# Optimization experiments

Hardware: AMD Instinct MI355X
Metric: run time of the kernel (lower is better)

Reference implementation:

```python
import jax, jax.numpy as jnp
import numpy as np

MAX_DELAY = 64   # kernel taps (module default 100; 64 = 4*block_size)
DT = 1.0
K_MIN = 0.1      # floor on storage constant for numerical safety


def _causal_depthwise_conv(x, k):
    """x: [B, C, T], k: [C, Tk].  y[b,c,t] = sum_tau k[c,tau] * x[b,c,t-tau]."""
    Tk = k.shape[1]
    return jax.lax.conv_general_dilated(
        x, k[:, None, ::-1], window_strides=(1,),
        padding=[(Tk - 1, 0)],
        feature_group_count=k.shape[0],
        dimension_numbers=('NCH', 'OIH', 'NCH'))


def _linear_storage_irf(params):
    """Per-node linear-reservoir impulse response, discretized to MAX_DELAY taps.
    params: [N, 2]; uses col 0 as (unconstrained) storage constant. -> [N, Tk]."""
    kst = jax.nn.softplus(params[:, 0]) + K_MIN              # [N]
    t = jnp.arange(MAX_DELAY, dtype=params.dtype) * DT       # [Tk]
    h = jnp.exp(-t[None, :] / kst[:, None]) * (DT / kst[:, None])
    return h / jnp.sum(h, axis=1, keepdims=True)             # unit mass


def setup_inputs() -> dict:
    key = jax.random.key(0)
    k1, k2, k3, k4 = jax.random.split(key, 4)
    B, N, T, E = 2, 4096, 2048, 8192
    x = jax.random.normal(k1, (B, N, T), dtype=jnp.float32)
    params = jax.random.normal(k2, (N, 2), dtype=jnp.float32)
    edge_src = jax.random.randint(k3, (E,), 0, N)
    edge_tgt = jax.random.randint(k4, (E,), 0, N)
    return {"x": x, "params": params, "edge_src": edge_src, "edge_tgt": edge_tgt}


def reference(x, params, edge_src, edge_tgt):
    B, N, T = x.shape
    # --- RoutingIRFAggregator: per-pair routing kernels ---
    h = _linear_storage_irf(params)                 # [N, Tk]
    h_src = h[edge_src]                             # [E, Tk] irregular gather
    h_tgt = h[edge_tgt]                             # [E, Tk]
    # edge kernel = causal composition (convolution) of src and tgt IRFs, truncated to Tk
    K_edge = _causal_depthwise_conv(h_src[None], h_tgt)[0]   # [E, Tk]
    # include diagonal (self) pairs since runoff_to_output=False
    K = jnp.concatenate([K_edge, h], axis=0)                 # [P, Tk], P = E + N
    src_all = jnp.concatenate([edge_src, jnp.arange(N)])
    tgt_all = jnp.concatenate([edge_tgt, jnp.arange(N)])
    # --- BlockSparseCausalConv: per-pair causal conv then scatter-add to targets ---
    xg = x[:, src_all, :]                           # [B, P, T] irregular gather
    yp = _causal_depthwise_conv(xg, K)              # [B, P, T]
    y = jax.ops.segment_sum(yp.transpose(1, 0, 2), tgt_all, num_segments=N)  # [N, B, T]
    return y.transpose(1, 0, 2)                     # [B, N, T]
```

## Files before the change

### kernel.cpp

```cpp
#include <hip/hip_runtime.h>
#include <math.h>

static constexpr int NN = 4096;
static constexpr int TT = 2048;
static constexpr int EE = 8192;
static constexpr int TK = 64;
static constexpr int CAP = 32;

typedef __attribute__((ext_vector_type(8))) short   short8v;
typedef __attribute__((ext_vector_type(4))) float   float4v;

__device__ __forceinline__ unsigned cvtpk_bf16(float lo, float hi) {
    unsigned r;
    asm("v_cvt_pk_bf16_f32 %0, %1, %2" : "=v"(r) : "v"(lo), "v"(hi));
    return r;
}

__global__ void irf_zero_kernel(const float* __restrict__ params,
                                float* __restrict__ hirf, int* __restrict__ cnt) {
    int blk = blockIdx.x;
    if (blk < 1024) {
        int t = blk * 256 + threadIdx.x;
        int node = t >> 6, lane = t & 63;
        float p = params[node * 2];
        float sp = fmaxf(p, 0.f) + log1pf(expf(-fabsf(p)));
        float kst = sp + 0.1f;
        float inv = 1.0f / kst;
        float hv = expf(-(float)lane * inv) * inv;
        float s = hv;
        #pragma unroll
        for (int d = 1; d < 64; d <<= 1) s += __shfl_xor(s, d, 64);
        hirf[node * TK + lane] = hv / s;
    } else {
        int i = (blk - 1024) * 256 + threadIdx.x;
        if (i < NN) cnt[i] = 0;
    }
}

__global__ void kedge_scatter_kernel(const float* __restrict__ hirf,
                                     const int* __restrict__ esrc, const int* __restrict__ etgt,
                                     float* __restrict__ Ke, int* __restrict__ cnt,
                                     int2* __restrict__ elist2) {
    __shared__ float s_src[4][TK];
    __shared__ float s_tgt[4][TK];
    int lane = threadIdx.x & 63;
    int grp  = threadIdx.x >> 6;
    int e = blockIdx.x * 4 + grp;
    int s = esrc[e], t = etgt[e];
    s_src[grp][lane] = hirf[s * TK + lane];
    s_tgt[grp][lane] = hirf[t * TK + lane];
    __syncthreads();
    float acc = 0.f;
    for (int tau = 0; tau <= lane; ++tau)
        acc += s_tgt[grp][tau] * s_src[grp][lane - tau];
    Ke[e * TK + lane] = acc;
    if (lane == 0) {
        int pos = atomicAdd(&cnt[t], 1);
        if (pos < CAP) elist2[t * CAP + pos] = make_int2(e, s);
    }
}

static constexpr int HALO = 80;
static constexpr int XLEN = HALO + TT;
static constexpr int TABS = 96;
static constexpr int TABE = TABS * 16;

struct __align__(16) ConvBuf {
    unsigned short x[XLEN];
    unsigned short tab[TABE];
};

__global__ __launch_bounds__(128)
void conv_mfma_kernel(const float* __restrict__ x,
                      const float* __restrict__ hirf, const float* __restrict__ Ke,
                      const int2* __restrict__ elist2,
                      const int* __restrict__ cnt,
                      float* __restrict__ y) {
    __shared__ ConvBuf sbuf[2];

    const int tid    = threadIdx.x;
    const int bid    = blockIdx.x;
    const int b      = bid & 1;
    const int tgt    = bid >> 1;
    const int l      = tid & 63;
    const int lane16 = l & 15;
    const int h      = l >> 4;
    const int hlo    = h & 1, hhi = h >> 1;
    const int half   = tid >> 6;

    for (int idx = tid; idx < 2 * HALO; idx += 128) {
        int nb = idx / HALO;
        sbuf[nb].x[idx % HALO] = 0;
    }
    {
        int z = tid & 15;
        #pragma unroll
        for (int rr = 0; rr < 2; ++rr) {
            int r2 = (tid >> 4) + 8 * rr;
            int c1 = z, c2 = (z <= r2) ? z + 16 : 80 + z;
            sbuf[0].tab[TABS * r2 + c1] = 0; sbuf[0].tab[TABS * r2 + c2] = 0;
            sbuf[1].tab[TABS * r2 + c1] = 0; sbuf[1].tab[TABS * r2 + c2] = 0;
        }
    }

    float4v acc[4];
    #pragma unroll
    for (int T = 0; T < 4; ++T) acc[T] = (float4v){0.f, 0.f, 0.f, 0.f};

    const float4* xbase = reinterpret_cast<const float4*>(x + (size_t)b * NN * TT);

    float4 pxA[4], pxB[4]; float pkA, pkB;

    auto LOAD_A = [&](int src, const float* Kp) {
        const float4* r0 = xbase + (size_t)src * (TT / 4);
        #pragma unroll
        for (int c = 0; c < 4; ++c) pxA[c] = r0[tid + 128 * c];
        pkA = Kp[l];
    };
    auto LOAD_B = [&](int src, const float* Kp) {
        const float4* r0 = xbase + (size_t)src * (TT / 4);
        #pragma unroll
        for (int c = 0; c < 4; ++c) pxB[c] = r0[tid + 128 * c];
        pkB = Kp[l];
    };
    auto WRITE_A = [&](int nb) {
        #pragma unroll
        for (int c = 0; c < 4; ++c) {
            int u = tid + 128 * c;
            unsigned lo = cvtpk_bf16(pxA[c].x, pxA[c].y);
            unsigned hi = cvtpk_bf16(pxA[c].z, pxA[c].w);
            *reinterpret_cast<uint2*>(&sbuf[nb].x[HALO + 4 * u]) = make_uint2(lo, hi);
        }
        unsigned short kb = (unsigned short)(cvtpk_bf16(pkA, pkA) & 0xffffu);
        int rg = tid >> 6;
        #pragma unroll
        for (int rr = 0; rr < 8; ++rr) {
            int r = rg * 8 + rr;
            sbuf[nb].tab[TABS * r + 80 + r - l] = kb;
        }
    };
    auto WRITE_B = [&](int nb) {
        #pragma unroll
        for (int c = 0; c < 4; ++c) {
            int u = tid + 128 * c;
            unsigned lo = cvtpk_bf16(pxB[c].x, pxB[c].y);
            unsigned hi = cvtpk_bf16(pxB[c].z, pxB[c].w);
            *reinterpret_cast<uint2*>(&sbuf[nb].x[HALO + 4 * u]) = make_uint2(lo, hi);
        }
        unsigned short kb = (unsigned short)(cvtpk_bf16(pkB, pkB) & 0xffffu);
        int rg = tid >> 6;
        #pragma unroll
        for (int rr = 0; rr < 8; ++rr) {
            int r = rg * 8 + rr;
            sbuf[nb].tab[TABS * r + 80 + r - l] = kb;
        }
    };
    auto COMPUTE = [&](int cb) {
        const unsigned short* tab = sbuf[cb].tab;
        const unsigned short* xb  = sbuf[cb].x;
        const int abase = TABS * lane16 + 80 + 8 * hlo;
        short8v A0 = *reinterpret_cast<const short8v*>(&tab[abase - 16 * (0 + hhi)]);
        short8v A1 = *reinterpret_cast<const short8v*>(&tab[abase - 16 * (2 + hhi)]);
        short8v A2 = *reinterpret_cast<const short8v*>(&tab[abase - 16 * (4 + hhi)]);
        #pragma unroll
        for (int T = 0; T < 4; ++T) {
            int bb = HALO + 16 * (64 * half + 16 * T + lane16) + 8 * hlo;
            short8v B0 = *reinterpret_cast<const short8v*>(&xb[bb - 16 * (0 + hhi)]);
            acc[T] = __builtin_amdgcn_mfma_f32_16x16x32_bf16(A0, B0, acc[T], 0, 0, 0);
            short8v B1 = *reinterpret_cast<const short8v*>(&xb[bb - 16 * (2 + hhi)]);
            acc[T] = __builtin_amdgcn_mfma_f32_16x16x32_bf16(A1, B1, acc[T], 0, 0, 0);
            short8v B2 = *reinterpret_cast<const short8v*>(&xb[bb - 16 * (4 + hhi)]);
            acc[T] = __builtin_amdgcn_mfma_f32_16x16x32_bf16(A2, B2, acc[T], 0, 0, 0);
        }
    };

    int deg = __builtin_amdgcn_readfirstlane(cnt[tgt]);
    if (deg > CAP) deg = CAP;
    const int nr = deg + 1;
    int mdE = 0, mdS = 0;

    LOAD_A(tgt, hirf + (size_t)tgt * TK);
    if (nr > 1) {
        int2 m = elist2[tgt * CAP];
        mdE = __builtin_amdgcn_readfirstlane(m.x);
        mdS = __builtin_amdgcn_readfirstlane(m.y);
        LOAD_B(mdS, Ke + (size_t)mdE * TK);
        if (nr > 2) {
            int2 m2 = elist2[tgt * CAP + 1];
            mdE = __builtin_amdgcn_readfirstlane(m2.x);
            mdS = __builtin_amdgcn_readfirstlane(m2.y);
        }
    }
    WRITE_A(0);
    __syncthreads();

    int i = 0;
    while (true) {
        if (i + 2 < nr) {
            LOAD_A(mdS, Ke + (size_t)mdE * TK);
            if (i + 3 < nr) {
                int2 m = elist2[tgt * CAP + i + 2];
                mdE = __builtin_amdgcn_readfirstlane(m.x);
                mdS = __builtin_amdgcn_readfirstlane(m.y);
            }
        }
        COMPUTE(0);
        if (i + 1 >= nr) break;
        WRITE_B(1);
        __syncthreads();
        ++i;
        if (i + 2 < nr) {
            LOAD_B(mdS, Ke + (size_t)mdE * TK);
            if (i + 3 < nr) {
                int2 m = elist2[tgt * CAP + i + 2];
                mdE = __builtin_amdgcn_readfirstlane(m.x);
                mdS = __builtin_amdgcn_readfirstlane(m.y);
            }
        }
        COMPUTE(1);
        if (i + 1 >= nr) break;
        WRITE_A(0);
        __syncthreads();
        ++i;
    }

    float* yrow = y + ((size_t)b * NN + tgt) * TT;
    #pragma unroll
    for (int T = 0; T < 4; ++T) {
        int tb = 16 * (64 * half + 16 * T + lane16) + 4 * h;
        float4v v = acc[T];
        __builtin_nontemporal_store(v, reinterpret_cast<float4v*>(yrow + tb));
    }
}

extern "C" void kernel_launch(void* const* d_in, const int* in_sizes, int n_in,
                              void* d_out, int out_size, void* d_ws, size_t ws_size,
                              hipStream_t stream) {
    const float* x      = (const float*)d_in[0];
    const float* params = (const float*)d_in[1];
    const int*   esrc   = (const int*)d_in[2];
    const int*   etgt   = (const int*)d_in[3];
    float* y = (float*)d_out;

    float* hirf = (float*)d_ws;
    float* Ke   = hirf + (size_t)NN * TK;
    int* cnt      = (int*)(Ke + (size_t)EE * TK);
    int2* elist2  = (int2*)(cnt + NN);

    hipLaunchKernelGGL(irf_zero_kernel, dim3(1040), dim3(256), 0, stream, params, hirf, cnt);
    hipLaunchKernelGGL(kedge_scatter_kernel, dim3(EE / 4), dim3(256), 0, stream,
                       hirf, esrc, etgt, Ke, cnt, elist2);
    hipLaunchKernelGGL(conv_mfma_kernel, dim3(NN * 2), dim3(128), 0, stream,
                       x, hirf, Ke, elist2, cnt, y);
}
```

Measured before the change: 53.85 us.

## Pre-convert x and kernels to bf16 in workspace before the gather conv

Adds a prep pass that converts all of x to bf16 in a workspace buffer, and stores the IRF and edge kernels as bf16. The conv kernel then gathers half-width rows and writes them straight to LDS without converting. Each source row is gathered about three times on average, so halving the gathered bytes is meant to cut memory traffic. The cost is an extra full read of x plus a write of the bf16 copy, and a fallback to fp32 loads if the workspace is too small.

```diff
diff --git a/kernel.cpp b/kernel.cpp
--- a/kernel.cpp
+++ b/kernel.cpp
@@ -7,8 +7,9 @@
 static constexpr int TK = 64;
 static constexpr int CAP = 32;
 
-typedef __attribute__((ext_vector_type(8))) short   short8v;
-typedef __attribute__((ext_vector_type(4))) float   float4v;
+typedef __attribute__((ext_vector_type(8))) short        short8v;
+typedef __attribute__((ext_vector_type(4))) float        float4v;
+typedef __attribute__((ext_vector_type(2))) unsigned int uint2v;
 
 __device__ __forceinline__ unsigned cvtpk_bf16(float lo, float hi) {
     unsigned r;
@@ -16,11 +17,24 @@
     return r;
 }
 
-__global__ void irf_zero_kernel(const float* __restrict__ params,
-                                float* __restrict__ hirf, int* __restrict__ cnt) {
+__global__ void prep_kernel(const float* __restrict__ params,
+                            const float* __restrict__ x,
+                            float* __restrict__ hirf, unsigned short* __restrict__ hb,
+                            unsigned short* __restrict__ xb, int* __restrict__ cnt,
+                            int doX) {
     int blk = blockIdx.x;
     if (blk < 1024) {
-        int t = blk * 256 + threadIdx.x;
+        if (!doX) return;
+        const float4* src = reinterpret_cast<const float4*>(x) + (size_t)blk * 4096 + threadIdx.x;
+        uint2v*       dst = reinterpret_cast<uint2v*>(xb) + (size_t)blk * 4096 + threadIdx.x;
+        #pragma unroll
+        for (int c = 0; c < 16; ++c) {
+            float4 v = src[c * 256];
+            uint2v o; o.x = cvtpk_bf16(v.x, v.y); o.y = cvtpk_bf16(v.z, v.w);
+            dst[c * 256] = o;
+        }
+    } else if (blk < 2048) {
+        int t = (blk - 1024) * 256 + threadIdx.x;
         int node = t >> 6, lane = t & 63;
         float p = params[node * 2];
         float sp = fmaxf(p, 0.f) + log1pf(expf(-fabsf(p)));
@@ -30,17 +44,19 @@
         float s = hv;
         #pragma unroll
         for (int d = 1; d < 64; d <<= 1) s += __shfl_xor(s, d, 64);
-        hirf[node * TK + lane] = hv / s;
+        float val = hv / s;
+        hirf[node * TK + lane] = val;
+        hb[node * TK + lane] = (unsigned short)(cvtpk_bf16(val, val) & 0xffffu);
     } else {
-        int i = (blk - 1024) * 256 + threadIdx.x;
+        int i = (blk - 2048) * 256 + threadIdx.x;
         if (i < NN) cnt[i] = 0;
     }
 }
 
-__global__ void kedge_scatter_kernel(const float* __restrict__ hirf,
-                                     const int* __restrict__ esrc, const int* __restrict__ etgt,
-                                     float* __restrict__ Ke, int* __restrict__ cnt,
-                                     int2* __restrict__ elist2) {
+__global__ void kedge_kernel(const float* __restrict__ hirf,
+                             const int* __restrict__ esrc, const int* __restrict__ etgt,
+                             unsigned short* __restrict__ Kb, int* __restrict__ cnt,
+                             int2* __restrict__ elist2) {
     __shared__ float s_src[4][TK];
     __shared__ float s_tgt[4][TK];
     int lane = threadIdx.x & 63;
@@ -53,7 +69,7 @@
     float acc = 0.f;
     for (int tau = 0; tau <= lane; ++tau)
         acc += s_tgt[grp][tau] * s_src[grp][lane - tau];
-    Ke[e * TK + lane] = acc;
+    Kb[e * TK + lane] = (unsigned short)(cvtpk_bf16(acc, acc) & 0xffffu);
     if (lane == 0) {
         int pos = atomicAdd(&cnt[t], 1);
         if (pos < CAP) elist2[t * CAP + pos] = make_int2(e, s);
@@ -70,9 +86,12 @@
     unsigned short tab[TABE];
 };
 
+template <int BF16X>
 __global__ __launch_bounds__(128)
-void conv_mfma_kernel(const float* __restrict__ x,
-                      const float* __restrict__ hirf, const float* __restrict__ Ke,
+void conv_mfma_kernel(const float* __restrict__ x32,
+                      const unsigned short* __restrict__ xb,
+                      const unsigned short* __restrict__ hb,
+                      const unsigned short* __restrict__ Kb,
                       const int2* __restrict__ elist2,
                       const int* __restrict__ cnt,
                       float* __restrict__ y) {
@@ -107,57 +126,75 @@
     #pragma unroll
     for (int T = 0; T < 4; ++T) acc[T] = (float4v){0.f, 0.f, 0.f, 0.f};
 
-    const float4* xbase = reinterpret_cast<const float4*>(x + (size_t)b * NN * TT);
-
-    float4 pxA[4], pxB[4]; float pkA, pkB;
-
-    auto LOAD_A = [&](int src, const float* Kp) {
-        const float4* r0 = xbase + (size_t)src * (TT / 4);
-        #pragma unroll
-        for (int c = 0; c < 4; ++c) pxA[c] = r0[tid + 128 * c];
+    float4  pxA32[4], pxB32[4];
+    short8v pxA16[2], pxB16[2];
+    unsigned short pkA, pkB;
+
+    auto LOAD_A = [&](int src, const unsigned short* Kp) {
+        if constexpr (BF16X) {
+            const short8v* r = reinterpret_cast<const short8v*>(xb + ((size_t)b * NN + src) * TT);
+            pxA16[0] = r[tid]; pxA16[1] = r[tid + 128];
+        } else {
+            const float4* r = reinterpret_cast<const float4*>(x32 + ((size_t)b * NN + src) * TT);
+            #pragma unroll
+            for (int c = 0; c < 4; ++c) pxA32[c] = r[tid + 128 * c];
+        }
         pkA = Kp[l];
     };
-    auto LOAD_B = [&](int src, const float* Kp) {
-        const float4* r0 = xbase + (size_t)src * (TT / 4);
-        #pragma unroll
-        for (int c = 0; c < 4; ++c) pxB[c] = r0[tid + 128 * c];
+    auto LOAD_B = [&](int src, const unsigned short* Kp) {
+        if constexpr (BF16X) {
+            const short8v* r = reinterpret_cast<const short8v*>(xb + ((size_t)b * NN + src) * TT);
+            pxB16[0] = r[tid]; pxB16[1] = r[tid + 128];
+        } else {
+            const float4* r = reinterpret_cast<const float4*>(x32 + ((size_t)b * NN + src) * TT);
+            #pragma unroll
+            for (int c = 0; c < 4; ++c) pxB32[c] = r[tid + 128 * c];
+        }
         pkB = Kp[l];
     };
     auto WRITE_A = [&](int nb) {
-        #pragma unroll
-        for (int c = 0; c < 4; ++c) {
-            int u = tid + 128 * c;
-            unsigned lo = cvtpk_bf16(pxA[c].x, pxA[c].y);
-            unsigned hi = cvtpk_bf16(pxA[c].z, pxA[c].w);
-            *reinterpret_cast<uint2*>(&sbuf[nb].x[HALO + 4 * u]) = make_uint2(lo, hi);
-        }
-        unsigned short kb = (unsigned short)(cvtpk_bf16(pkA, pkA) & 0xffffu);
+        if constexpr (BF16X) {
+            *reinterpret_cast<short8v*>(&sbuf[nb].x[HALO + 8 * tid])         = pxA16[0];
+            *reinterpret_cast<short8v*>(&sbuf[nb].x[HALO + 8 * (tid + 128)]) = pxA16[1];
+        } else {
+            #pragma unroll
+            for (int c = 0; c < 4; ++c) {
+                int u = tid + 128 * c;
+                unsigned lo = cvtpk_bf16(pxA32[c].x, pxA32[c].y);
+                unsigned hi = cvtpk_bf16(pxA32[c].z, pxA32[c].w);
+                *reinterpret_cast<uint2*>(&sbuf[nb].x[HALO + 4 * u]) = make_uint2(lo, hi);
+            }
+        }
         int rg = tid >> 6;
         #pragma unroll
         for (int rr = 0; rr < 8; ++rr) {
             int r = rg * 8 + rr;
-            sbuf[nb].tab[TABS * r + 80 + r - l] = kb;
+            sbuf[nb].tab[TABS * r + 80 + r - l] = pkA;
         }
     };
     auto WRITE_B = [&](int nb) {
-        #pragma unroll
-        for (int c = 0; c < 4; ++c) {
-            int u = tid + 128 * c;
-            unsigned lo = cvtpk_bf16(pxB[c].x, pxB[c].y);
-            unsigned hi = cvtpk_bf16(pxB[c].z, pxB[c].w);
-            *reinterpret_cast<uint2*>(&sbuf[nb].x[HALO + 4 * u]) = make_uint2(lo, hi);
-        }
-        unsigned short kb = (unsigned short)(cvtpk_bf16(pkB, pkB) & 0xffffu);
+        if constexpr (BF16X) {
+            *reinterpret_cast<short8v*>(&sbuf[nb].x[HALO + 8 * tid])         = pxB16[0];
+            *reinterpret_cast<short8v*>(&sbuf[nb].x[HALO + 8 * (tid + 128)]) = pxB16[1];
+        } else {
+            #pragma unroll
+            for (int c = 0; c < 4; ++c) {
+                int u = tid + 128 * c;
+                unsigned lo = cvtpk_bf16(pxB32[c].x, pxB32[c].y);
+                unsigned hi = cvtpk_bf16(pxB32[c].z, pxB32[c].w);
+                *reinterpret_cast<uint2*>(&sbuf[nb].x[HALO + 4 * u]) = make_uint2(lo, hi);
+            }
+        }
         int rg = tid >> 6;
         #pragma unroll
         for (int rr = 0; rr < 8; ++rr) {
             int r = rg * 8 + rr;
-            sbuf[nb].tab[TABS * r + 80 + r - l] = kb;
+            sbuf[nb].tab[TABS * r + 80 + r - l] = pkB;
         }
     };
     auto COMPUTE = [&](int cb) {
         const unsigned short* tab = sbuf[cb].tab;
-        const unsigned short* xb  = sbuf[cb].x;
+        const unsigned short* xv  = sbuf[cb].x;
         const int abase = TABS * lane16 + 80 + 8 * hlo;
         short8v A0 = *reinterpret_cast<const short8v*>(&tab[abase - 16 * (0 + hhi)]);
         short8v A1 = *reinterpret_cast<const short8v*>(&tab[abase - 16 * (2 + hhi)]);
@@ -165,11 +202,11 @@
         #pragma unroll
         for (int T = 0; T < 4; ++T) {
             int bb = HALO + 16 * (64 * half + 16 * T + lane16) + 8 * hlo;
-            short8v B0 = *reinterpret_cast<const short8v*>(&xb[bb - 16 * (0 + hhi)]);
+            short8v B0 = *reinterpret_cast<const short8v*>(&xv[bb - 16 * (0 + hhi)]);
             acc[T] = __builtin_amdgcn_mfma_f32_16x16x32_bf16(A0, B0, acc[T], 0, 0, 0);
-            short8v B1 = *reinterpret_cast<const short8v*>(&xb[bb - 16 * (2 + hhi)]);
+            short8v B1 = *reinterpret_cast<const short8v*>(&xv[bb - 16 * (2 + hhi)]);
             acc[T] = __builtin_amdgcn_mfma_f32_16x16x32_bf16(A1, B1, acc[T], 0, 0, 0);
-            short8v B2 = *reinterpret_cast<const short8v*>(&xb[bb - 16 * (4 + hhi)]);
+            short8v B2 = *reinterpret_cast<const short8v*>(&xv[bb - 16 * (4 + hhi)]);
             acc[T] = __builtin_amdgcn_mfma_f32_16x16x32_bf16(A2, B2, acc[T], 0, 0, 0);
         }
     };
@@ -179,12 +216,12 @@
     const int nr = deg + 1;
     int mdE = 0, mdS = 0;
 
-    LOAD_A(tgt, hirf + (size_t)tgt * TK);
+    LOAD_A(tgt, hb + (size_t)tgt * TK);
     if (nr > 1) {
         int2 m = elist2[tgt * CAP];
         mdE = __builtin_amdgcn_readfirstlane(m.x);
         mdS = __builtin_amdgcn_readfirstlane(m.y);
-        LOAD_B(mdS, Ke + (size_t)mdE * TK);
+        LOAD_B(mdS, Kb + (size_t)mdE * TK);
         if (nr > 2) {
             int2 m2 = elist2[tgt * CAP + 1];
             mdE = __builtin_amdgcn_readfirstlane(m2.x);
@@ -197,7 +234,7 @@
     int i = 0;
     while (true) {
         if (i + 2 < nr) {
-            LOAD_A(mdS, Ke + (size_t)mdE * TK);
+            LOAD_A(mdS, Kb + (size_t)mdE * TK);
             if (i + 3 < nr) {
                 int2 m = elist2[tgt * CAP + i + 2];
                 mdE = __builtin_amdgcn_readfirstlane(m.x);
@@ -210,7 +247,7 @@
         __syncthreads();
         ++i;
         if (i + 2 < nr) {
-            LOAD_B(mdS, Ke + (size_t)mdE * TK);
+            LOAD_B(mdS, Kb + (size_t)mdE * TK);
             if (i + 3 < nr) {
                 int2 m = elist2[tgt * CAP + i + 2];
                 mdE = __builtin_amdgcn_readfirstlane(m.x);
@@ -242,14 +279,26 @@
     const int*   etgt   = (const int*)d_in[3];
     float* y = (float*)d_out;
 
-    float* hirf = (float*)d_ws;
-    float* Ke   = hirf + (size_t)NN * TK;
-    int* cnt      = (int*)(Ke + (size_t)EE * TK);
-    int2* elist2  = (int2*)(cnt + NN);
-
-    hipLaunchKernelGGL(irf_zero_kernel, dim3(1040), dim3(256), 0, stream, params, hirf, cnt);
-    hipLaunchKernelGGL(kedge_scatter_kernel, dim3(EE / 4), dim3(256), 0, stream,
-                       hirf, esrc, etgt, Ke, cnt, elist2);
-    hipLaunchKernelGGL(conv_mfma_kernel, dim3(NN * 2), dim3(128), 0, stream,
-                       x, hirf, Ke, elist2, cnt, y);
-}
+    char* w = (char*)d_ws;
+    float*          hirf   = (float*)w;          w += (size_t)NN * TK * 4;
+    unsigned short* hb     = (unsigned short*)w; w += (size_t)NN * TK * 2;
+    unsigned short* Kb     = (unsigned short*)w; w += (size_t)EE * TK * 2;
+    int*            cnt    = (int*)w;            w += (size_t)NN * 4;
+    int2*           elist2 = (int2*)w;           w += (size_t)NN * CAP * 8;
+    unsigned short* xb     = (unsigned short*)w; w += (size_t)2 * NN * TT * 2;
+
+    size_t need = (size_t)(w - (char*)d_ws);
+    int doX = (ws_size >= need) ? 1 : 0;
+
+    hipLaunchKernelGGL(prep_kernel, dim3(2064), dim3(256), 0, stream,
+                       params, x, hirf, hb, xb, cnt, doX);
+    hipLaunchKernelGGL(kedge_kernel, dim3(EE / 4), dim3(256), 0, stream,
+                       hirf, esrc, etgt, Kb, cnt, elist2);
+    if (doX) {
+        hipLaunchKernelGGL((conv_mfma_kernel<1>), dim3(NN * 2), dim3(128), 0, stream,
+                           x, xb, hb, Kb, elist2, cnt, y);
+    } else {
+        hipLaunchKernelGGL((conv_mfma_kernel<0>), dim3(NN * 2), dim3(128), 0, stream,
+                           x, xb, hb, Kb, elist2, cnt, y);
+    }
+}
```

Measured after the change: 52.52 us. 1.03x faster.
